# Kernel optimization log

Measured on AMD Instinct MI355X. Metric: run time of the kernel, lower is better.

The kernel has to match this reference:

```python
import jax, jax.numpy as jnp
import numpy as np

N_NEIGHBORS = 16
N_CLASSES = 10

def setup_inputs() -> dict:
    key = jax.random.key(0)
    k1, k2, k3 = jax.random.split(key, 3)
    x = jax.random.normal(k1, (1024, 64), dtype=jnp.float32)
    train_data = jax.random.normal(k2, (100000, 64), dtype=jnp.float32)
    train_labels = jax.random.randint(k3, (100000,), 0, N_CLASSES, dtype=jnp.int64)
    return {"x": x, "train_data": train_data, "train_labels": train_labels}

def reference(x, train_data, train_labels):
    # Pairwise L2 distances [B, N] via the quadratic expansion (same math as cdist p=2)
    x2 = jnp.sum(x * x, axis=-1, keepdims=True)            # [B, 1]
    t2 = jnp.sum(train_data * train_data, axis=-1)          # [N]
    d2 = x2 - 2.0 * (x @ train_data.T) + t2                 # [B, N]
    dist = jnp.sqrt(jnp.maximum(d2, 0.0))
    # k smallest distances
    neg_d, idx = jax.lax.top_k(-dist, N_NEIGHBORS)           # [B, k]
    d = -neg_d
    labels = train_labels[idx]                               # [B, k] gather
    # weights = 'distance': inverse distance, with exact-match rows handled
    w = 1.0 / d
    inf_mask = jnp.isinf(w)
    inf_row = jnp.any(inf_mask, axis=1, keepdims=True)
    w = jnp.where(inf_row, inf_mask.astype(w.dtype), w)
    # scatter_add weighted votes into [B, C]
    B = x.shape[0]
    rows = jnp.arange(B)[:, None]
    proba = jnp.zeros((B, N_CLASSES), dtype=w.dtype).at[rows, labels].add(w)
    s = jnp.sum(proba, axis=1, keepdims=True)
    s = jnp.where(s == 0.0, jnp.float32(1.0), s)
    proba = proba / s
    return jnp.argmax(proba, axis=1), proba
```

## Files before the change

kernel.cpp:

```cpp
#include <hip/hip_runtime.h>
#include <math.h>


constexpr int D        = 64;
constexpr int K        = 16;
constexpr int NCLS     = 10;
constexpr int CHUNKLEN = 1024;
constexpr int NCHUNK   = 104;
constexpr int NPAD     = NCHUNK * 1024 + 64;
constexpr int NSUB     = 64;
constexpr int SUBLEN   = 128;
constexpr int SLOT     = 16;
constexpr int MSEL     = 48;
constexpr int SGPTS    = 32;
constexpr int SGBYTES  = SGPTS * 128;
constexpr int SLOTB    = SGBYTES + 256;
constexpr int NCVT     = (NPAD * 4) / 256;

typedef __attribute__((ext_vector_type(8))) short bf16x8_t;
typedef __attribute__((ext_vector_type(4))) float f32x4_t;
typedef unsigned short ushort_t;

__device__ __forceinline__ ushort_t f32_to_bf16_rne(float f) {
  unsigned int u = __float_as_uint(f);
  unsigned int r = u + 0x7FFFu + ((u >> 16) & 1u);
  return (ushort_t)(r >> 16);
}

__device__ __forceinline__ bf16x8_t pack_bf16x8(float4 a, float4 b) {
  union { ushort_t u[8]; bf16x8_t v; } r;
  r.u[0] = f32_to_bf16_rne(a.x); r.u[1] = f32_to_bf16_rne(a.y);
  r.u[2] = f32_to_bf16_rne(a.z); r.u[3] = f32_to_bf16_rne(a.w);
  r.u[4] = f32_to_bf16_rne(b.x); r.u[5] = f32_to_bf16_rne(b.y);
  r.u[6] = f32_to_bf16_rne(b.z); r.u[7] = f32_to_bf16_rne(b.w);
  return r.v;
}

__device__ __forceinline__ void glds16(const void* g, void* l) {
  __builtin_amdgcn_global_load_lds(
      (const __attribute__((address_space(1))) void*)g,
      (__attribute__((address_space(3))) void*)l, 16, 0, 0);
}
__device__ __forceinline__ void glds4(const void* g, void* l) {
  __builtin_amdgcn_global_load_lds(
      (const __attribute__((address_space(1))) void*)g,
      (__attribute__((address_space(3))) void*)l, 4, 0, 0);
}

__global__ __launch_bounds__(256) void knn_prep(
    const float* __restrict__ train, const float* __restrict__ x,
    ushort_t* __restrict__ tb, float* __restrict__ t2,
    float* __restrict__ nt2h, float* __restrict__ samp, int N)
{
  __shared__ float nh_l[4][16];
  const int tid = threadIdx.x;

  if ((int)blockIdx.x < NCVT) {
    int gid = blockIdx.x * 256 + tid;
    int row = gid >> 2, qt = gid & 3;
    ushort_t* dst = tb + (size_t)row * D + qt * 16;
    if (row >= N) {
      uint2 z = make_uint2(0u, 0u);
      #pragma unroll
      for (int i = 0; i < 4; ++i) *reinterpret_cast<uint2*>(dst + i * 4) = z;
      if (qt == 0) { t2[row] = INFINITY; nt2h[row] = -INFINITY; }
      return;
    }
    const float* src = train + (size_t)row * D + qt * 16;
    float nrm = 0.f;
    #pragma unroll
    for (int i = 0; i < 4; ++i) {
      float4 v = *reinterpret_cast<const float4*>(src + i * 4);
      nrm = fmaf(v.x, v.x, nrm); nrm = fmaf(v.y, v.y, nrm);
      nrm = fmaf(v.z, v.z, nrm); nrm = fmaf(v.w, v.w, nrm);
      uint2 hh = make_uint2(
        (unsigned)f32_to_bf16_rne(v.x) | ((unsigned)f32_to_bf16_rne(v.y) << 16),
        (unsigned)f32_to_bf16_rne(v.z) | ((unsigned)f32_to_bf16_rne(v.w) << 16));
      *reinterpret_cast<uint2*>(dst + i * 4) = hh;
    }
    nrm += __shfl_xor(nrm, 1);
    nrm += __shfl_xor(nrm, 2);
    if (qt == 0) { t2[row] = nrm; nt2h[row] = -0.5f * nrm; }
    return;
  }

  const int bid2 = blockIdx.x - NCVT;
  const int w = tid >> 6, lane = tid & 63;
  const int lh = lane & 15, lg = lane >> 4;
  const int qb = bid2 & 15, sub = bid2 >> 4;
  const int q = qb * 64 + w * 16 + lh;

  const float* xrp = x + (size_t)q * D + lg * 8;
  bf16x8_t B0 = pack_bf16x8(*reinterpret_cast<const float4*>(xrp),
                            *reinterpret_cast<const float4*>(xrp + 4));
  bf16x8_t B1 = pack_bf16x8(*reinterpret_cast<const float4*>(xrp + 32),
                            *reinterpret_cast<const float4*>(xrp + 36));

  float Ld[4] = {-INFINITY, -INFINITY, -INFINITY, -INFINITY};
  const int pstart = sub * SUBLEN;

  for (int j = 0; j < SUBLEN / 16; ++j) {
    const float* tr = train + (size_t)(pstart + j * 16 + lh) * D;
    float4 f0 = *reinterpret_cast<const float4*>(tr + lg * 8);
    float4 f1 = *reinterpret_cast<const float4*>(tr + lg * 8 + 4);
    float4 f2 = *reinterpret_cast<const float4*>(tr + 32 + lg * 8);
    float4 f3 = *reinterpret_cast<const float4*>(tr + 32 + lg * 8 + 4);
    bf16x8_t A0 = pack_bf16x8(f0, f1);
    bf16x8_t A1 = pack_bf16x8(f2, f3);
    float pn = 0.f;
    pn = fmaf(f0.x, f0.x, pn); pn = fmaf(f0.y, f0.y, pn);
    pn = fmaf(f0.z, f0.z, pn); pn = fmaf(f0.w, f0.w, pn);
    pn = fmaf(f1.x, f1.x, pn); pn = fmaf(f1.y, f1.y, pn);
    pn = fmaf(f1.z, f1.z, pn); pn = fmaf(f1.w, f1.w, pn);
    pn = fmaf(f2.x, f2.x, pn); pn = fmaf(f2.y, f2.y, pn);
    pn = fmaf(f2.z, f2.z, pn); pn = fmaf(f2.w, f2.w, pn);
    pn = fmaf(f3.x, f3.x, pn); pn = fmaf(f3.y, f3.y, pn);
    pn = fmaf(f3.z, f3.z, pn); pn = fmaf(f3.w, f3.w, pn);
    pn += __shfl_xor(pn, 16);
    pn += __shfl_xor(pn, 32);
    if (lg == 0) nh_l[w][lh] = -0.5f * pn;
    float4 nh = *reinterpret_cast<const float4*>(&nh_l[w][lg * 4]);
    f32x4_t c = {nh.x, nh.y, nh.z, nh.w};
    c = __builtin_amdgcn_mfma_f32_16x16x32_bf16(A0, B0, c, 0, 0, 0);
    c = __builtin_amdgcn_mfma_f32_16x16x32_bf16(A1, B1, c, 0, 0, 0);
    #pragma unroll
    for (int r = 0; r < 4; ++r) {
      float sv = c[r];
      if (sv > Ld[3]) {
        Ld[3] = sv;
        if (Ld[3] > Ld[2]) { float s_ = Ld[3]; Ld[3] = Ld[2]; Ld[2] = s_; }
        if (Ld[2] > Ld[1]) { float s_ = Ld[2]; Ld[2] = Ld[1]; Ld[1] = s_; }
        if (Ld[1] > Ld[0]) { float s_ = Ld[1]; Ld[1] = Ld[0]; Ld[0] = s_; }
      }
    }
  }

  float* outp = samp + (size_t)q * (NSUB * 16) + sub * 16 + lg * 4;
  *reinterpret_cast<float4*>(outp) = make_float4(Ld[0], Ld[1], Ld[2], Ld[3]);
}

__global__ __launch_bounds__(256) void knn_theta(
    const float* __restrict__ samp, float* __restrict__ theta, int B)
{
  const int w = threadIdx.x >> 6, lane = threadIdx.x & 63;
  const int q = blockIdx.x * 4 + w;
  if (q >= B) return;

  const float* s = samp + (size_t)q * (NSUB * 16) + lane * 16;
  float4 p0 = *reinterpret_cast<const float4*>(s);
  float4 p1 = *reinterpret_cast<const float4*>(s + 4);
  float4 p2 = *reinterpret_cast<const float4*>(s + 8);
  float4 p3 = *reinterpret_cast<const float4*>(s + 12);
  float L0[4] = {p0.x, p0.y, p0.z, p0.w};
  float L1[4] = {p1.x, p1.y, p1.z, p1.w};
  float L2[4] = {p2.x, p2.y, p2.z, p2.w};
  float L3[4] = {p3.x, p3.y, p3.z, p3.w};

  float th = -INFINITY;
  for (int r = 0; r < K; ++r) {
    float bd = fmaxf(fmaxf(L0[0], L1[0]), fmaxf(L2[0], L3[0]));
    #pragma unroll
    for (int sdx = 0; sdx < 6; ++sdx) bd = fmaxf(bd, __shfl_xor(bd, 32 >> sdx));
    if (L0[0] == bd) { L0[0] = L0[1]; L0[1] = L0[2]; L0[2] = L0[3]; L0[3] = -INFINITY; }
    if (L1[0] == bd) { L1[0] = L1[1]; L1[1] = L1[2]; L1[2] = L1[3]; L1[3] = -INFINITY; }
    if (L2[0] == bd) { L2[0] = L2[1]; L2[1] = L2[2]; L2[2] = L2[3]; L2[3] = -INFINITY; }
    if (L3[0] == bd) { L3[0] = L3[1]; L3[1] = L3[2]; L3[2] = L3[3]; L3[3] = -INFINITY; }
    th = bd;
  }
  if (lane == 0) theta[q] = th;
}

__global__ __launch_bounds__(256) void knn_filter(
    const ushort_t* __restrict__ tb, const float* __restrict__ x,
    const float* __restrict__ nt2h, const float* __restrict__ theta,
    int* __restrict__ cnts, int2* __restrict__ cand2)
{
  __shared__ char ring[4][2][SLOTB];
  __shared__ int  cnt_l[64];
  __shared__ int2 list_p[64][SLOT];

  const int tid = threadIdx.x;
  const int w = tid >> 6, lane = tid & 63;
  const int lh = lane & 15, lg = lane >> 4;

  const int d   = blockIdx.x + 16 * blockIdx.y;
  const int xcd = d & 7;
  const int t_  = d >> 3;
  const int qb  = t_ & 15;
  const int ch  = ((t_ >> 4) << 3) | xcd;

  const int q0  = qb * 64;
  const int wp0 = ch * CHUNKLEN + w * 256;

  if (tid < 64) cnt_l[tid] = 0;
  __syncthreads();

  bf16x8_t Bq0[4], Bq1[4];
  float th[4];
  #pragma unroll
  for (int ct = 0; ct < 4; ++ct) {
    const float* xrp = x + (size_t)(q0 + ct * 16 + lh) * D + lg * 8;
    Bq0[ct] = pack_bf16x8(*reinterpret_cast<const float4*>(xrp),
                          *reinterpret_cast<const float4*>(xrp + 4));
    Bq1[ct] = pack_bf16x8(*reinterpret_cast<const float4*>(xrp + 32),
                          *reinterpret_cast<const float4*>(xrp + 36));
    th[ct] = theta[q0 + ct * 16 + lh];
  }

  char* myring = &ring[w][0][0];
  const char*  gA = (const char*)(tb + (size_t)wp0 * D);
  const float* gN = nt2h + wp0;
  const int rowoff = (lane >> 3) * 128;
  const int swz    = (((lane & 7) ^ (lane >> 3)) << 4);
  const int lhx    = lh & 7;

  #define ISSUE(SG)                                                              \
    {                                                                            \
      char* sb = myring + (((SG) & 1) ? SLOTB : 0);                              \
      const char* ga = gA + (size_t)(SG) * SGBYTES;                              \
      glds16(ga + rowoff + swz,        sb);                                      \
      glds16(ga + 1024 + rowoff + swz, sb + 1024);                               \
      glds16(ga + 2048 + rowoff + swz, sb + 2048);                               \
      glds16(ga + 3072 + rowoff + swz, sb + 3072);                               \
      glds4 (gN + (SG) * SGPTS + lane, sb + 4096);                               \
    }

  #define COMPUTE(SG)                                                            \
    {                                                                            \
      const char* sb = myring + (((SG) & 1) ? SLOTB : 0);                        \
      _Pragma("unroll")                                                          \
      for (int g2 = 0; g2 < 2; ++g2) {                                           \
        bf16x8_t A0 = *reinterpret_cast<const bf16x8_t*>(                        \
            sb + g2 * 2048 + lh * 128 + ((lg ^ lhx) << 4));                      \
        bf16x8_t A1 = *reinterpret_cast<const bf16x8_t*>(                        \
            sb + g2 * 2048 + lh * 128 + (((lg + 4) ^ lhx) << 4));                \
        float4 nh = *reinterpret_cast<const float4*>(                            \
            sb + 4096 + g2 * 64 + lg * 16);                                      \
        const int pg = wp0 + (SG) * SGPTS + g2 * 16 + lg * 4;                    \
        _Pragma("unroll")                                                        \
        for (int ct = 0; ct < 4; ++ct) {                                         \
          f32x4_t c = {nh.x, nh.y, nh.z, nh.w};                                  \
          c = __builtin_amdgcn_mfma_f32_16x16x32_bf16(A0, Bq0[ct], c, 0, 0, 0);  \
          c = __builtin_amdgcn_mfma_f32_16x16x32_bf16(A1, Bq1[ct], c, 0, 0, 0);  \
          float mx = fmaxf(fmaxf(c[0], c[1]), fmaxf(c[2], c[3]));                \
          if (mx >= th[ct]) {                                                    \
            const int qloc = ct * 16 + lh;                                       \
            _Pragma("unroll")                                                    \
            for (int r = 0; r < 4; ++r) {                                        \
              if (c[r] >= th[ct]) {                                              \
                int pos = atomicAdd(&cnt_l[qloc], 1);                            \
                if (pos < SLOT)                                                  \
                  list_p[qloc][pos] = make_int2(pg + r, __float_as_int(c[r]));   \
              }                                                                  \
            }                                                                    \
          }                                                                      \
        }                                                                        \
      }                                                                          \
    }

  asm volatile("s_waitcnt vmcnt(0)" ::: "memory");
  ISSUE(0);
  #pragma unroll
  for (int it = 0; it < 8; ++it) {
    if (it < 7) {
      ISSUE(it + 1);
      asm volatile("s_waitcnt vmcnt(5)" ::: "memory");
    } else {
      asm volatile("s_waitcnt vmcnt(0)" ::: "memory");
    }
    COMPUTE(it);
  }
  #undef ISSUE
  #undef COMPUTE

  __syncthreads();
  if (tid < 64) {
    int n = cnt_l[tid]; if (n > SLOT) n = SLOT;
    size_t o = (size_t)(q0 + tid) * NCHUNK + ch;
    cnts[o] = n;
    for (int j = 0; j < n; ++j) cand2[o * SLOT + j] = list_p[tid][j];
  }
}

__global__ __launch_bounds__(256) void knn_vote(
    const float* __restrict__ x, const float* __restrict__ train,
    const float* __restrict__ t2, const int* __restrict__ labels,
    const int* __restrict__ cnts, const int2* __restrict__ cand2,
    float* __restrict__ out, int B, int N)
{
  __shared__ int2  cpair[NCHUNK * SLOT + 4];
  __shared__ float sortd[MSEL];
  __shared__ int   sorti[MSEL];
  __shared__ float xs[D];
  __shared__ int   total_s;
  __shared__ float x2_s;

  const int tid = threadIdx.x;
  const int w = tid >> 6, lane = tid & 63;
  const int q = blockIdx.x;

  if (tid == 0) total_s = 0;
  if (tid < D) xs[tid] = x[(size_t)q * D + tid];
  if (tid < MSEL) { sortd[tid] = INFINITY; sorti[tid] = 0x7fffffff; }
  __syncthreads();

  if (w == 0) {
    float v = xs[lane];
    float s = v * v;
    #pragma unroll
    for (int o = 32; o > 0; o >>= 1) s += __shfl_xor(s, o);
    if (lane == 0) x2_s = s;
  }
  if (tid < NCHUNK) {
    int n = cnts[(size_t)q * NCHUNK + tid];
    int base = atomicAdd(&total_s, n);
    const int2* src = cand2 + ((size_t)q * NCHUNK + tid) * SLOT;
    for (int j = 0; j < n; ++j) cpair[base + j] = src[j];
  }
  __syncthreads();

  const int total = total_s;
  const int totalPad = (total + 3) & ~3;
  const float x2 = x2_s;
  if (tid < totalPad - total)
    cpair[total + tid] = make_int2(0x7fffffff, __float_as_int(-INFINITY));
  __syncthreads();

  for (int j = tid; j < total; j += 256) {
    int2 mine = cpair[j];
    float ms = __int_as_float(mine.y);
    int   mi = mine.x;
    int rank = 0;
    for (int k = 0; k < totalPad; k += 4) {
      int2 o0 = cpair[k];     int2 o1 = cpair[k + 1];
      int2 o2 = cpair[k + 2]; int2 o3 = cpair[k + 3];
      float s0 = __int_as_float(o0.y), s1 = __int_as_float(o1.y);
      float s2 = __int_as_float(o2.y), s3 = __int_as_float(o3.y);
      rank += ((s0 > ms || (s0 == ms && o0.x < mi)) ? 1 : 0)
            + ((s1 > ms || (s1 == ms && o1.x < mi)) ? 1 : 0)
            + ((s2 > ms || (s2 == ms && o2.x < mi)) ? 1 : 0)
            + ((s3 > ms || (s3 == ms && o3.x < mi)) ? 1 : 0);
    }
    if (rank < MSEL) { sortd[rank] = ms; sorti[rank] = mi; }
  }
  __syncthreads();

  if (tid < MSEL * 4) {
    const int ci = tid >> 2, qt = tid & 3;
    const int idx = sorti[ci];
    float dot = 0.f;
    if (idx != 0x7fffffff) {
      const float* tr = train + (size_t)idx * D + qt * 16;
      #pragma unroll
      for (int i = 0; i < 4; ++i) {
        float4 tv = *reinterpret_cast<const float4*>(tr + i * 4);
        dot = fmaf(xs[qt * 16 + i * 4 + 0], tv.x, dot);
        dot = fmaf(xs[qt * 16 + i * 4 + 1], tv.y, dot);
        dot = fmaf(xs[qt * 16 + i * 4 + 2], tv.z, dot);
        dot = fmaf(xs[qt * 16 + i * 4 + 3], tv.w, dot);
      }
    }
    dot += __shfl_xor(dot, 1);
    dot += __shfl_xor(dot, 2);
    if (qt == 0)
      sortd[ci] = (idx != 0x7fffffff)
                ? fmaxf(x2 - 2.f * dot + t2[idx], 0.f) : INFINITY;
  }
  __syncthreads();

  if (w == 0) {
    float vd = (lane < MSEL) ? sortd[lane] : INFINITY;
    int   vi = (lane < MSEL) ? sorti[lane] : 0x7fffffff;
    float myD = INFINITY; int myI = 0;
    for (int r = 0; r < K; ++r) {
      float bd = vd; int bi = vi;
      #pragma unroll
      for (int s = 0; s < 6; ++s) {
        int off = 32 >> s;
        float od = __shfl_xor(bd, off);
        int   oi = __shfl_xor(bi, off);
        if (od < bd || (od == bd && oi < bi)) { bd = od; bi = oi; }
      }
      if (vd == bd && vi == bi) { vd = INFINITY; vi = 0x7fffffff; }
      if (lane == r) { myD = bd; myI = bi; }
    }

    int valid = (lane < K) && (myD < INFINITY) && (myI < N);
    float dist = sqrtf(fmaxf(myD, 0.f));
    int lab = labels[(valid && myI < N) ? myI : 0];
    int isz = (valid && dist == 0.f) ? 1 : 0;
    float wgt = 1.f / dist;

    float accw[NCLS]; float acci[NCLS]; int anyInf = 0;
    #pragma unroll
    for (int c = 0; c < NCLS; ++c) { accw[c] = 0.f; acci[c] = 0.f; }
    for (int r = 0; r < K; ++r) {
      int   vr   = __shfl(valid, r);
      int   labr = __shfl(lab, r);
      float wgtr = __shfl(wgt, r);
      int   iszr = __shfl(isz, r);
      if (vr) {
        anyInf |= iszr;
        #pragma unroll
        for (int c = 0; c < NCLS; ++c) {
          accw[c] += (labr == c) ? wgtr : 0.f;
          acci[c] += (labr == c && iszr) ? 1.f : 0.f;
        }
      }
    }

    if (lane == 0) {
      float proba[NCLS]; float s = 0.f;
      #pragma unroll
      for (int c = 0; c < NCLS; ++c) { proba[c] = anyInf ? acci[c] : accw[c]; s += proba[c]; }
      if (s == 0.f) s = 1.f;
      #pragma unroll
      for (int c = 0; c < NCLS; ++c) proba[c] = proba[c] / s;
      int best = 0; float bv = proba[0];
      #pragma unroll
      for (int c = 1; c < NCLS; ++c) if (proba[c] > bv) { bv = proba[c]; best = c; }
      out[q] = (float)best;
      #pragma unroll
      for (int c = 0; c < NCLS; ++c) out[B + q * NCLS + c] = proba[c];
    }
  }
}

extern "C" void kernel_launch(void* const* d_in, const int* in_sizes, int n_in,
                              void* d_out, int out_size, void* d_ws, size_t ws_size,
                              hipStream_t stream)
{
  const float* x      = (const float*)d_in[0];
  const float* train  = (const float*)d_in[1];
  const int*   labels = (const int*)d_in[2];
  float* out = (float*)d_out;

  const int B = in_sizes[0] / D;
  const int N = in_sizes[2];

  char* ws = (char*)d_ws;
  size_t off = 0;
  ushort_t* train_bf = (ushort_t*)(ws + off); off += (size_t)NPAD * D * 2;
  float*    t2       = (float*)(ws + off);    off += (size_t)NPAD * 4;
  float*    nt2h     = (float*)(ws + off);    off += (size_t)NPAD * 4;
  float*    theta    = (float*)(ws + off);    off += (size_t)B * 4;
  int*      cnts     = (int*)(ws + off);      off += (size_t)B * NCHUNK * 4;
  int2*     cand2    = (int2*)(ws + off);     off += (size_t)B * NCHUNK * SLOT * 8;
  float*    samp     = (float*)cand2;

  knn_prep<<<NCVT + (B / 64) * NSUB, 256, 0, stream>>>(train, x, train_bf, t2, nt2h, samp, N);
  knn_theta<<<(B + 3) / 4, 256, 0, stream>>>(samp, theta, B);
  knn_filter<<<dim3(16, NCHUNK), 256, 0, stream>>>(train_bf, x, nt2h, theta, cnts, cand2);
  knn_vote<<<B, 256, 0, stream>>>(x, train, t2, labels, cnts, cand2, out, B, N);
}
```

Measured before the change: 105.6 us.

## Split train conversion from sampling and fuse sample top-k with theta reduction

```diff
diff --git a/kernel.cpp b/kernel.cpp
--- a/kernel.cpp
+++ b/kernel.cpp
@@ -8,14 +8,12 @@
 constexpr int CHUNKLEN = 1024;
 constexpr int NCHUNK   = 104;
 constexpr int NPAD     = NCHUNK * 1024 + 64;
-constexpr int NSUB     = 64;
-constexpr int SUBLEN   = 128;
+constexpr int NSAMP    = 8192;
 constexpr int SLOT     = 16;
 constexpr int MSEL     = 48;
 constexpr int SGPTS    = 32;
 constexpr int SGBYTES  = SGPTS * 128;
 constexpr int SLOTB    = SGBYTES + 256;
-constexpr int NCVT     = (NPAD * 4) / 256;
 
 typedef __attribute__((ext_vector_type(8))) short bf16x8_t;
 typedef __attribute__((ext_vector_type(4))) float f32x4_t;
@@ -47,48 +45,49 @@
       (__attribute__((address_space(3))) void*)l, 4, 0, 0);
 }
 
-__global__ __launch_bounds__(256) void knn_prep(
-    const float* __restrict__ train, const float* __restrict__ x,
-    ushort_t* __restrict__ tb, float* __restrict__ t2,
-    float* __restrict__ nt2h, float* __restrict__ samp, int N)
+__global__ __launch_bounds__(256) void cvt_train(
+    const float* __restrict__ t, ushort_t* __restrict__ tb,
+    float* __restrict__ t2, float* __restrict__ nt2h, int N)
 {
-  __shared__ float nh_l[4][16];
+  int gid = blockIdx.x * 256 + threadIdx.x;
+  int row = gid >> 2, qt = gid & 3;
+  if (row >= NPAD) return;
+  ushort_t* dst = tb + (size_t)row * D + qt * 16;
+  if (row >= N) {
+    uint2 z = make_uint2(0u, 0u);
+    #pragma unroll
+    for (int i = 0; i < 4; ++i) *reinterpret_cast<uint2*>(dst + i * 4) = z;
+    if (qt == 0) { t2[row] = INFINITY; nt2h[row] = -INFINITY; }
+    return;
+  }
+  const float* src = t + (size_t)row * D + qt * 16;
+  float nrm = 0.f;
+  #pragma unroll
+  for (int i = 0; i < 4; ++i) {
+    float4 v = *reinterpret_cast<const float4*>(src + i * 4);
+    nrm = fmaf(v.x, v.x, nrm); nrm = fmaf(v.y, v.y, nrm);
+    nrm = fmaf(v.z, v.z, nrm); nrm = fmaf(v.w, v.w, nrm);
+    uint2 hh = make_uint2(
+      (unsigned)f32_to_bf16_rne(v.x) | ((unsigned)f32_to_bf16_rne(v.y) << 16),
+      (unsigned)f32_to_bf16_rne(v.z) | ((unsigned)f32_to_bf16_rne(v.w) << 16));
+    *reinterpret_cast<uint2*>(dst + i * 4) = hh;
+  }
+  nrm += __shfl_xor(nrm, 1);
+  nrm += __shfl_xor(nrm, 2);
+  if (qt == 0) { t2[row] = nrm; nt2h[row] = -0.5f * nrm; }
+}
+
+__global__ __launch_bounds__(256) void knn_sample_theta(
+    const ushort_t* __restrict__ tb, const float* __restrict__ x,
+    const float* __restrict__ nt2h, float* __restrict__ theta)
+{
+  __shared__ float4 lists[16][16];
+
   const int tid = threadIdx.x;
-
-  if ((int)blockIdx.x < NCVT) {
-    int gid = blockIdx.x * 256 + tid;
-    int row = gid >> 2, qt = gid & 3;
-    ushort_t* dst = tb + (size_t)row * D + qt * 16;
-    if (row >= N) {
-      uint2 z = make_uint2(0u, 0u);
-      #pragma unroll
-      for (int i = 0; i < 4; ++i) *reinterpret_cast<uint2*>(dst + i * 4) = z;
-      if (qt == 0) { t2[row] = INFINITY; nt2h[row] = -INFINITY; }
-      return;
-    }
-    const float* src = train + (size_t)row * D + qt * 16;
-    float nrm = 0.f;
-    #pragma unroll
-    for (int i = 0; i < 4; ++i) {
-      float4 v = *reinterpret_cast<const float4*>(src + i * 4);
-      nrm = fmaf(v.x, v.x, nrm); nrm = fmaf(v.y, v.y, nrm);
-      nrm = fmaf(v.z, v.z, nrm); nrm = fmaf(v.w, v.w, nrm);
-      uint2 hh = make_uint2(
-        (unsigned)f32_to_bf16_rne(v.x) | ((unsigned)f32_to_bf16_rne(v.y) << 16),
-        (unsigned)f32_to_bf16_rne(v.z) | ((unsigned)f32_to_bf16_rne(v.w) << 16));
-      *reinterpret_cast<uint2*>(dst + i * 4) = hh;
-    }
-    nrm += __shfl_xor(nrm, 1);
-    nrm += __shfl_xor(nrm, 2);
-    if (qt == 0) { t2[row] = nrm; nt2h[row] = -0.5f * nrm; }
-    return;
-  }
-
-  const int bid2 = blockIdx.x - NCVT;
   const int w = tid >> 6, lane = tid & 63;
   const int lh = lane & 15, lg = lane >> 4;
-  const int qb = bid2 & 15, sub = bid2 >> 4;
-  const int q = qb * 64 + w * 16 + lh;
+  const int q0 = blockIdx.x * 16;
+  const int q = q0 + lh;
 
   const float* xrp = x + (size_t)q * D + lg * 8;
   bf16x8_t B0 = pack_bf16x8(*reinterpret_cast<const float4*>(xrp),
@@ -97,29 +96,14 @@
                             *reinterpret_cast<const float4*>(xrp + 36));
 
   float Ld[4] = {-INFINITY, -INFINITY, -INFINITY, -INFINITY};
-  const int pstart = sub * SUBLEN;
-
-  for (int j = 0; j < SUBLEN / 16; ++j) {
-    const float* tr = train + (size_t)(pstart + j * 16 + lh) * D;
-    float4 f0 = *reinterpret_cast<const float4*>(tr + lg * 8);
-    float4 f1 = *reinterpret_cast<const float4*>(tr + lg * 8 + 4);
-    float4 f2 = *reinterpret_cast<const float4*>(tr + 32 + lg * 8);
-    float4 f3 = *reinterpret_cast<const float4*>(tr + 32 + lg * 8 + 4);
-    bf16x8_t A0 = pack_bf16x8(f0, f1);
-    bf16x8_t A1 = pack_bf16x8(f2, f3);
-    float pn = 0.f;
-    pn = fmaf(f0.x, f0.x, pn); pn = fmaf(f0.y, f0.y, pn);
-    pn = fmaf(f0.z, f0.z, pn); pn = fmaf(f0.w, f0.w, pn);
-    pn = fmaf(f1.x, f1.x, pn); pn = fmaf(f1.y, f1.y, pn);
-    pn = fmaf(f1.z, f1.z, pn); pn = fmaf(f1.w, f1.w, pn);
-    pn = fmaf(f2.x, f2.x, pn); pn = fmaf(f2.y, f2.y, pn);
-    pn = fmaf(f2.z, f2.z, pn); pn = fmaf(f2.w, f2.w, pn);
-    pn = fmaf(f3.x, f3.x, pn); pn = fmaf(f3.y, f3.y, pn);
-    pn = fmaf(f3.z, f3.z, pn); pn = fmaf(f3.w, f3.w, pn);
-    pn += __shfl_xor(pn, 16);
-    pn += __shfl_xor(pn, 32);
-    if (lg == 0) nh_l[w][lh] = -0.5f * pn;
-    float4 nh = *reinterpret_cast<const float4*>(&nh_l[w][lg * 4]);
+  const int pstart = w * (NSAMP / 4);
+
+  #pragma unroll 4
+  for (int j = 0; j < (NSAMP / 4) / 16; ++j) {
+    const ushort_t* ap = tb + (size_t)(pstart + j * 16 + lh) * D + lg * 8;
+    bf16x8_t A0 = *reinterpret_cast<const bf16x8_t*>(ap);
+    bf16x8_t A1 = *reinterpret_cast<const bf16x8_t*>(ap + 32);
+    float4 nh = *reinterpret_cast<const float4*>(nt2h + pstart + j * 16 + lg * 4);
     f32x4_t c = {nh.x, nh.y, nh.z, nh.w};
     c = __builtin_amdgcn_mfma_f32_16x16x32_bf16(A0, B0, c, 0, 0, 0);
     c = __builtin_amdgcn_mfma_f32_16x16x32_bf16(A1, B1, c, 0, 0, 0);
@@ -135,39 +119,25 @@
     }
   }
 
-  float* outp = samp + (size_t)q * (NSUB * 16) + sub * 16 + lg * 4;
-  *reinterpret_cast<float4*>(outp) = make_float4(Ld[0], Ld[1], Ld[2], Ld[3]);
-}
-
-__global__ __launch_bounds__(256) void knn_theta(
-    const float* __restrict__ samp, float* __restrict__ theta, int B)
-{
-  const int w = threadIdx.x >> 6, lane = threadIdx.x & 63;
-  const int q = blockIdx.x * 4 + w;
-  if (q >= B) return;
-
-  const float* s = samp + (size_t)q * (NSUB * 16) + lane * 16;
-  float4 p0 = *reinterpret_cast<const float4*>(s);
-  float4 p1 = *reinterpret_cast<const float4*>(s + 4);
-  float4 p2 = *reinterpret_cast<const float4*>(s + 8);
-  float4 p3 = *reinterpret_cast<const float4*>(s + 12);
-  float L0[4] = {p0.x, p0.y, p0.z, p0.w};
-  float L1[4] = {p1.x, p1.y, p1.z, p1.w};
-  float L2[4] = {p2.x, p2.y, p2.z, p2.w};
-  float L3[4] = {p3.x, p3.y, p3.z, p3.w};
-
-  float th = -INFINITY;
-  for (int r = 0; r < K; ++r) {
-    float bd = fmaxf(fmaxf(L0[0], L1[0]), fmaxf(L2[0], L3[0]));
-    #pragma unroll
-    for (int sdx = 0; sdx < 6; ++sdx) bd = fmaxf(bd, __shfl_xor(bd, 32 >> sdx));
-    if (L0[0] == bd) { L0[0] = L0[1]; L0[1] = L0[2]; L0[2] = L0[3]; L0[3] = -INFINITY; }
-    if (L1[0] == bd) { L1[0] = L1[1]; L1[1] = L1[2]; L1[2] = L1[3]; L1[3] = -INFINITY; }
-    if (L2[0] == bd) { L2[0] = L2[1]; L2[1] = L2[2]; L2[2] = L2[3]; L2[3] = -INFINITY; }
-    if (L3[0] == bd) { L3[0] = L3[1]; L3[1] = L3[2]; L3[2] = L3[3]; L3[3] = -INFINITY; }
-    th = bd;
-  }
-  if (lane == 0) theta[q] = th;
+  lists[lh][w * 4 + lg] = make_float4(Ld[0], Ld[1], Ld[2], Ld[3]);
+  __syncthreads();
+
+  {
+    const int mq = w * 4 + lg;
+    float4 v = lists[mq][lh];
+    float L[4] = {v.x, v.y, v.z, v.w};
+    float th = -INFINITY;
+    for (int r = 0; r < K; ++r) {
+      float bd = L[0];
+      bd = fmaxf(bd, __shfl_xor(bd, 1));
+      bd = fmaxf(bd, __shfl_xor(bd, 2));
+      bd = fmaxf(bd, __shfl_xor(bd, 4));
+      bd = fmaxf(bd, __shfl_xor(bd, 8));
+      if (L[0] == bd) { L[0] = L[1]; L[1] = L[2]; L[2] = L[3]; L[3] = -INFINITY; }
+      th = bd;
+    }
+    if (lh == 0) theta[q0 + mq] = th;
+  }
 }
 
 __global__ __launch_bounds__(256) void knn_filter(
@@ -446,10 +416,9 @@
   float*    theta    = (float*)(ws + off);    off += (size_t)B * 4;
   int*      cnts     = (int*)(ws + off);      off += (size_t)B * NCHUNK * 4;
   int2*     cand2    = (int2*)(ws + off);     off += (size_t)B * NCHUNK * SLOT * 8;
-  float*    samp     = (float*)cand2;
-
-  knn_prep<<<NCVT + (B / 64) * NSUB, 256, 0, stream>>>(train, x, train_bf, t2, nt2h, samp, N);
-  knn_theta<<<(B + 3) / 4, 256, 0, stream>>>(samp, theta, B);
+
+  cvt_train<<<(NPAD * 4 + 255) / 256, 256, 0, stream>>>(train, train_bf, t2, nt2h, N);
+  knn_sample_theta<<<B / 16, 256, 0, stream>>>(train_bf, x, nt2h, theta);
   knn_filter<<<dim3(16, NCHUNK), 256, 0, stream>>>(train_bf, x, nt2h, theta, cnts, cand2);
   knn_vote<<<B, 256, 0, stream>>>(x, train, t2, labels, cnts, cand2, out, B, N);
 }
```

After: 164.1 us. +55.4%, slower.
